# Kernel optimization log

Measured on AMD Instinct MI355X. Metric: run time of the kernel, lower is better.

Reference implementation:

```python
import jax, jax.numpy as jnp
import numpy as np

QMAX = 127.0

def fake_quant(x):
    # per-tensor symmetric int8 fake quantize-dequantize (QAT)
    s = jnp.maximum(jnp.max(jnp.abs(x)) / QMAX, 1e-8)
    q = jnp.clip(jnp.round(x / s), -QMAX, QMAX) * s
    return x + jax.lax.stop_gradient(q - x)  # STE

def qlinear(x, w, b):
    # x already fake-quantized by caller (input_quantizer); weights fake-quantized here
    return jnp.einsum('btc,oc->bto', x, fake_quant(w)) + b

def layer_norm(x, g, b, eps=1e-5):
    m = jnp.mean(x, axis=-1, keepdims=True)
    v = jnp.var(x, axis=-1, keepdims=True)
    return (x - m) * jax.lax.rsqrt(v + eps) * g + b

def setup_inputs() -> dict:
    key = jax.random.key(0)
    ks = jax.random.split(key, 8)
    B, T, C, I = 8, 512, 1024, 4096
    sd = 0.02
    return {
        'hidden_states': jax.random.normal(ks[0], (B, T, C), jnp.float32),
        'attention_mask': jnp.ones((B, T), jnp.float32),
        'ln1_g': jnp.ones((C,), jnp.float32), 'ln1_b': jnp.zeros((C,), jnp.float32),
        'ln2_g': jnp.ones((C,), jnp.float32), 'ln2_b': jnp.zeros((C,), jnp.float32),
        'w_qkv': sd * jax.random.normal(ks[1], (3 * C, C), jnp.float32),
        'b_qkv': jnp.zeros((3 * C,), jnp.float32),
        'w_out': sd * jax.random.normal(ks[2], (C, C), jnp.float32),
        'b_out': jnp.zeros((C,), jnp.float32),
        'w1': sd * jax.random.normal(ks[3], (I, C), jnp.float32),
        'b1': jnp.zeros((I,), jnp.float32),
        'w2': sd * jax.random.normal(ks[4], (C, I), jnp.float32),
        'b2': jnp.zeros((C,), jnp.float32),
    }

def reference(hidden_states, attention_mask, ln1_g, ln1_b, ln2_g, ln2_b,
              w_qkv, b_qkv, w_out, b_out, w1, b1, w2, b2):
    B, T, C = hidden_states.shape
    H = 16
    Dh = C // H
    scale = Dh ** -0.5

    # --- attention branch (pre-norm) ---
    x = layer_norm(hidden_states, ln1_g, ln1_b)
    qkv = qlinear(fake_quant(x), w_qkv, b_qkv)            # [B,T,3C]
    qkv = qkv.reshape(B, T, 3, H, Dh).transpose(2, 0, 3, 1, 4)
    q, k, v = qkv[0], qkv[1], qkv[2]                       # [B,H,T,Dh]
    scores = jnp.einsum('bhqd,bhkd->bhqk', q, k) * scale
    ext = (1.0 - attention_mask)[:, None, None, :] * -10000.0
    scores = scores + ext
    attn = jax.nn.softmax(scores, axis=-1)
    out = jnp.einsum('bhqk,bhkd->bhqd', attn, v)
    out = out.transpose(0, 2, 1, 3).reshape(B, T, C)
    attn_out = qlinear(fake_quant(out), w_out, b_out)
    h = hidden_states + attn_out

    # --- MLP branch (pre-norm) ---
    x = layer_norm(h, ln2_g, ln2_b)
    x = qlinear(fake_quant(x), w1, b1)
    x = jax.nn.gelu(x, approximate=False)
    x = qlinear(fake_quant(x), w2, b2)
    return h + x
```

## Files before the change

### kernel.cpp

```cpp
#include <hip/hip_runtime.h>

typedef __attribute__((ext_vector_type(8))) short bf16x8;
typedef __attribute__((ext_vector_type(4))) float f32x4;
typedef __attribute__((ext_vector_type(4))) int i32x4;
typedef unsigned short u16;
typedef unsigned int u32;

#define B_ 8
#define T_ 512
#define C_ 1024
#define I_ 4096
#define H_ 16
#define Dh_ 64
#define BT (B_*T_)
#define NH (B_*H_)

__device__ __forceinline__ float bf2f(u16 u) {
  return __uint_as_float(((u32)u) << 16);
}
__device__ __forceinline__ u16 f2bf(float f) {
  u32 u = __float_as_uint(f);
  u32 r = u + 0x7FFFu + ((u >> 16) & 1u);
  return (u16)(r >> 16);
}
__device__ __forceinline__ float wredMax(float v) {
#pragma unroll
  for (int o = 32; o; o >>= 1) v = fmaxf(v, __shfl_xor(v, o));
  return v;
}
__device__ __forceinline__ float wredSum(float v) {
#pragma unroll
  for (int o = 32; o; o >>= 1) v += __shfl_xor(v, o);
  return v;
}
__device__ __forceinline__ void slotAtomicMax(u32* arr, int bid, float bm) {
  u32 b = __float_as_uint(bm);
  volatile u32* p = arr + ((bid & 63) << 4);
  if (b > *p) atomicMax((u32*)p, b);
}
__device__ __forceinline__ float slotMax(const u32* __restrict__ arr) {
  float m = 0.f;
#pragma unroll
  for (int i = 0; i < 64; ++i) m = fmaxf(m, __uint_as_float(arr[i << 4]));
  return m;
}
__device__ __forceinline__ void gload16(const void* g, void* l) {
  __builtin_amdgcn_global_load_lds((const __attribute__((address_space(1))) void*)g,
                                   (__attribute__((address_space(3))) void*)l, 16, 0, 0);
}
__device__ __forceinline__ int qi(float v, float inv) {
  return (int)fminf(fmaxf(rintf(v * inv), -127.f), 127.f);
}
__device__ __forceinline__ float gelu1(float v) {
  float x2 = v * v;
  float e = __expf(v * fmaf(-0.0713548755f, x2, -1.5957691216f));
  return v * __builtin_amdgcn_rcpf(1.0f + e);
}

__global__ void k_init(u32* s) {
  int i = blockIdx.x * 256 + threadIdx.x;
  if (i < 8192) s[i] = 0u;
}

__global__ __launch_bounds__(256) void k_pre1(
    const float* __restrict__ p0, int n0,
    const float* __restrict__ p1, int n1,
    const float* __restrict__ p2, int n2,
    const float* __restrict__ p3, int n3,
    u32* __restrict__ scw,
    const float* __restrict__ x, const float* __restrict__ g,
    const float* __restrict__ b, u16* __restrict__ y,
    u32* __restrict__ arr) {
  const int t = threadIdx.x;
  if (blockIdx.x < 512) {
    int stride = 512 * 256;
    int gid = blockIdx.x * 256 + t;
    float m0 = 0.f, m1 = 0.f, m2 = 0.f, m3 = 0.f;
    for (int i = gid; i < n0; i += stride) {
      float4 v = ((const float4*)p0)[i];
      m0 = fmaxf(m0, fmaxf(fmaxf(fabsf(v.x), fabsf(v.y)), fmaxf(fabsf(v.z), fabsf(v.w))));
    }
    for (int i = gid; i < n1; i += stride) {
      float4 v = ((const float4*)p1)[i];
      m1 = fmaxf(m1, fmaxf(fmaxf(fabsf(v.x), fabsf(v.y)), fmaxf(fabsf(v.z), fabsf(v.w))));
    }
    for (int i = gid; i < n2; i += stride) {
      float4 v = ((const float4*)p2)[i];
      m2 = fmaxf(m2, fmaxf(fmaxf(fabsf(v.x), fabsf(v.y)), fmaxf(fabsf(v.z), fabsf(v.w))));
    }
    for (int i = gid; i < n3; i += stride) {
      float4 v = ((const float4*)p3)[i];
      m3 = fmaxf(m3, fmaxf(fmaxf(fabsf(v.x), fabsf(v.y)), fmaxf(fabsf(v.z), fabsf(v.w))));
    }
    m0 = wredMax(m0); m1 = wredMax(m1); m2 = wredMax(m2); m3 = wredMax(m3);
    __shared__ float red4[4][4];
    int wid = t >> 6, lane = t & 63;
    if (lane == 0) { red4[wid][0] = m0; red4[wid][1] = m1; red4[wid][2] = m2; red4[wid][3] = m3; }
    __syncthreads();
    if (t < 4) {
      int j = t;
      float bm = fmaxf(fmaxf(red4[0][j], red4[1][j]), fmaxf(red4[2][j], red4[3][j]));
      slotAtomicMax(scw + j * 1024, blockIdx.x, bm);
    }
  } else {
    int row = blockIdx.x - 512;
    float4 v = ((const float4*)(x + (long)row * C_))[t];
    float s1 = v.x + v.y + v.z + v.w;
    float s2 = v.x * v.x + v.y * v.y + v.z * v.z + v.w * v.w;
    s1 = wredSum(s1);
    s2 = wredSum(s2);
    __shared__ float red[8];
    int wid = t >> 6, lane = t & 63;
    if (lane == 0) { red[wid] = s1; red[4 + wid] = s2; }
    __syncthreads();
    s1 = red[0] + red[1] + red[2] + red[3];
    s2 = red[4] + red[5] + red[6] + red[7];
    float mean = s1 * (1.0f / C_);
    float var = s2 * (1.0f / C_) - mean * mean;
    float inv = rsqrtf(var + 1e-5f);
    float4 gv = ((const float4*)g)[t];
    float4 bv = ((const float4*)b)[t];
    float4 o;
    o.x = (v.x - mean) * inv * gv.x + bv.x;
    o.y = (v.y - mean) * inv * gv.y + bv.y;
    o.z = (v.z - mean) * inv * gv.z + bv.z;
    o.w = (v.w - mean) * inv * gv.w + bv.w;
    ushort4 ob;
    ob.x = f2bf(o.x); ob.y = f2bf(o.y); ob.z = f2bf(o.z); ob.w = f2bf(o.w);
    ((ushort4*)(y + (long)row * C_))[t] = ob;
    float m = fmaxf(fmaxf(fabsf(o.x), fabsf(o.y)), fmaxf(fabsf(o.z), fabsf(o.w)));
    m = wredMax(m);
    __syncthreads();
    if (lane == 0) red[wid] = m;
    __syncthreads();
    if (t == 0) {
      float bm = fmaxf(fmaxf(red[0], red[1]), fmaxf(red[2], red[3]));
      slotAtomicMax(arr, row, bm);
    }
  }
}

__global__ __launch_bounds__(256) void k_pre2(
    const float* __restrict__ p0, signed char* __restrict__ q0, int n0,
    const float* __restrict__ p1, signed char* __restrict__ q1, int n1,
    const float* __restrict__ p2, signed char* __restrict__ q2, int n2,
    const float* __restrict__ p3, signed char* __restrict__ q3, int n3,
    const u32* __restrict__ scw,
    const u16* __restrict__ xb, signed char* __restrict__ xq, int n8,
    const u32* __restrict__ arrX) {
  const int t = threadIdx.x;
  if (blockIdx.x < 512) {
    int stride = 512 * 256;
    int gid = blockIdx.x * 256 + t;
#define QLOOP(p, q, n, slot)                                                        \
    {                                                                               \
      float s = fmaxf(slotMax(scw + slot * 1024) * (1.0f / 127.0f), 1e-8f);         \
      float inv = 1.0f / s;                                                         \
      for (int i = gid; i < n; i += stride) {                                       \
        float4 v = ((const float4*)p)[i];                                           \
        u32 pk = (u32)(qi(v.x, inv) & 255) | ((u32)(qi(v.y, inv) & 255) << 8) |     \
                 ((u32)(qi(v.z, inv) & 255) << 16) | ((u32)(qi(v.w, inv) & 255) << 24); \
        ((u32*)q)[i] = pk;                                                          \
      }                                                                             \
    }
    QLOOP(p0, q0, n0, 0)
    QLOOP(p1, q1, n1, 1)
    QLOOP(p2, q2, n2, 2)
    QLOOP(p3, q3, n3, 3)
#undef QLOOP
  } else {
    float s = fmaxf(slotMax(arrX) * (1.0f / 127.0f), 1e-8f);
    float inv = 1.0f / s;
    int stride = 512 * 256;
    for (int i = (blockIdx.x - 512) * 256 + t; i < n8; i += stride) {
      uint4 d = ((const uint4*)xb)[i];
      u16* e = (u16*)&d;
      uint2 o;
      o.x = (u32)(qi(bf2f(e[0]), inv) & 255) | ((u32)(qi(bf2f(e[1]), inv) & 255) << 8) |
            ((u32)(qi(bf2f(e[2]), inv) & 255) << 16) | ((u32)(qi(bf2f(e[3]), inv) & 255) << 24);
      o.y = (u32)(qi(bf2f(e[4]), inv) & 255) | ((u32)(qi(bf2f(e[5]), inv) & 255) << 8) |
            ((u32)(qi(bf2f(e[6]), inv) & 255) << 16) | ((u32)(qi(bf2f(e[7]), inv) & 255) << 24);
      ((uint2*)xq)[i] = o;
    }
  }
}

__global__ __launch_bounds__(256) void k_quant_b8(const u16* __restrict__ x, signed char* __restrict__ q,
                                                  int n8, const u32* __restrict__ arr) {
  float s = fmaxf(slotMax(arr) * (1.0f / 127.0f), 1e-8f);
  float inv = 1.0f / s;
  int stride = gridDim.x * blockDim.x;
  for (int i = blockIdx.x * blockDim.x + threadIdx.x; i < n8; i += stride) {
    uint4 d = ((const uint4*)x)[i];
    u16* e = (u16*)&d;
    uint2 o;
    o.x = (u32)(qi(bf2f(e[0]), inv) & 255) | ((u32)(qi(bf2f(e[1]), inv) & 255) << 8) |
          ((u32)(qi(bf2f(e[2]), inv) & 255) << 16) | ((u32)(qi(bf2f(e[3]), inv) & 255) << 24);
    o.y = (u32)(qi(bf2f(e[4]), inv) & 255) | ((u32)(qi(bf2f(e[5]), inv) & 255) << 8) |
          ((u32)(qi(bf2f(e[6]), inv) & 255) << 16) | ((u32)(qi(bf2f(e[7]), inv) & 255) << 24);
    ((uint2*)q)[i] = o;
  }
}

__global__ __launch_bounds__(256) void k_lnb(const u16* __restrict__ x, const float* __restrict__ g,
                                             const float* __restrict__ b, u16* __restrict__ y,
                                             u32* __restrict__ arr) {
  int row = blockIdx.x;
  int t = threadIdx.x;
  ushort4 xb = ((const ushort4*)(x + (long)row * C_))[t];
  float4 v;
  v.x = bf2f(xb.x); v.y = bf2f(xb.y); v.z = bf2f(xb.z); v.w = bf2f(xb.w);
  float s1 = v.x + v.y + v.z + v.w;
  float s2 = v.x * v.x + v.y * v.y + v.z * v.z + v.w * v.w;
  s1 = wredSum(s1);
  s2 = wredSum(s2);
  __shared__ float red[8];
  int wid = t >> 6, lane = t & 63;
  if (lane == 0) { red[wid] = s1; red[4 + wid] = s2; }
  __syncthreads();
  s1 = red[0] + red[1] + red[2] + red[3];
  s2 = red[4] + red[5] + red[6] + red[7];
  float mean = s1 * (1.0f / C_);
  float var = s2 * (1.0f / C_) - mean * mean;
  float inv = rsqrtf(var + 1e-5f);
  float4 gv = ((const float4*)g)[t];
  float4 bv = ((const float4*)b)[t];
  float4 o;
  o.x = (v.x - mean) * inv * gv.x + bv.x;
  o.y = (v.y - mean) * inv * gv.y + bv.y;
  o.z = (v.z - mean) * inv * gv.z + bv.z;
  o.w = (v.w - mean) * inv * gv.w + bv.w;
  ushort4 ob;
  ob.x = f2bf(o.x); ob.y = f2bf(o.y); ob.z = f2bf(o.z); ob.w = f2bf(o.w);
  ((ushort4*)(y + (long)row * C_))[t] = ob;
  float m = fmaxf(fmaxf(fabsf(o.x), fabsf(o.y)), fmaxf(fabsf(o.z), fabsf(o.w)));
  m = wredMax(m);
  __syncthreads();
  if (lane == 0) red[wid] = m;
  __syncthreads();
  if (t == 0) {
    float bm = fmaxf(fmaxf(red[0], red[1]), fmaxf(red[2], red[3]));
    slotAtomicMax(arr, row, bm);
  }
}

__global__ __launch_bounds__(256, 1) void k_attn(
    const u16* __restrict__ qkv, const float* __restrict__ mask,
    u16* __restrict__ O, u32* __restrict__ amax) {
  __shared__ u16 Ke[512 * 64];
  __shared__ u16 Vt[64 * 512];
  __shared__ u16 Pl[4 * 64 * 40];
  __shared__ float extl[512];
  __shared__ float redm[4];
  const int tid = threadIdx.x;
  const int w = tid >> 6, l = tid & 63;
  const int head = blockIdx.x;
  const int chunk = blockIdx.y;
  const int b = head >> 4, h = head & 15;
  const long rowbase = (long)(b * 512) * (3 * C_);

  {
    const u16* Kg = qkv + rowbase + C_ + h * 64;
    int lr8 = l >> 3;
    int ls = (l & 7) ^ lr8;
    const long koff = (long)lr8 * (3 * C_) + ls * 8;
#pragma unroll
    for (int i = 0; i < 16; ++i) {
      int r0 = w * 128 + i * 8;
      gload16(Kg + (long)r0 * (3 * C_) + koff, &Ke[r0 * 64]);
    }
  }
  {
    const u16* Vg = qkv + rowbase + 2 * C_ + h * 64;
    int kvl = tid & 31;
    int d0 = (tid >> 5) * 8;
#pragma unroll 4
    for (int i = 0; i < 16; ++i) {
      int kv = i * 32 + kvl;
      uint4 t4 = *(const uint4*)(Vg + (long)kv * (3 * C_) + d0);
      u16* tv = (u16*)&t4;
      int slot = kv >> 3, within = kv & 7;
#pragma unroll
      for (int j = 0; j < 8; ++j) {
        int d = d0 + j;
        Vt[d * 512 + ((slot ^ (d & 7)) << 3) + within] = tv[j];
      }
    }
  }
  {
    const float* mb = mask + b * 512;
    extl[tid] = (1.0f - mb[tid]) * -10000.0f;
    extl[tid + 256] = (1.0f - mb[tid + 256]) * -10000.0f;
  }
  const int qbase = chunk * 256 + w * 64;
  bf16x8 qf[4][2];
  {
    const u16* Qg = qkv + rowbase + h * 64;
#pragma unroll
    for (int qt = 0; qt < 4; ++qt)
#pragma unroll
      for (int dc = 0; dc < 2; ++dc)
        qf[qt][dc] = *(const bf16x8*)(Qg + (long)(qbase + qt * 16 + (l & 15)) * (3 * C_) + dc * 32 + (l >> 4) * 8);
  }
  __syncthreads();

  f32x4 oacc[4][4];
  float mrun[4], lrun[4];
#pragma unroll
  for (int qt = 0; qt < 4; ++qt) { mrun[qt] = -3.0e38f; lrun[qt] = 0.f; }
#pragma unroll
  for (int dt = 0; dt < 4; ++dt)
#pragma unroll
    for (int qt = 0; qt < 4; ++qt) oacc[dt][qt] = (f32x4){0.f, 0.f, 0.f, 0.f};

  u16* Pw = &Pl[w * 64 * 40];

  for (int ks = 0; ks < 16; ++ks) {
    bf16x8 kf[2][2];
#pragma unroll
    for (int kvt = 0; kvt < 2; ++kvt) {
      int kv = ks * 32 + kvt * 16 + (l & 15);
#pragma unroll
      for (int dc = 0; dc < 2; ++dc) {
        int phys = (dc * 4 + (l >> 4)) ^ (kv & 7);
        kf[kvt][dc] = *(const bf16x8*)&Ke[kv * 64 + phys * 8];
      }
    }
    f32x4 sacc[2][4];
#pragma unroll
    for (int kvt = 0; kvt < 2; ++kvt)
#pragma unroll
      for (int qt = 0; qt < 4; ++qt) {
        f32x4 a = (f32x4){0.f, 0.f, 0.f, 0.f};
        a = __builtin_amdgcn_mfma_f32_16x16x32_bf16(kf[kvt][0], qf[qt][0], a, 0, 0, 0);
        a = __builtin_amdgcn_mfma_f32_16x16x32_bf16(kf[kvt][1], qf[qt][1], a, 0, 0, 0);
        sacc[kvt][qt] = a;
      }
#pragma unroll
    for (int kvt = 0; kvt < 2; ++kvt) {
      f32x4 ev = *(const f32x4*)&extl[ks * 32 + kvt * 16 + (l >> 4) * 4];
#pragma unroll
      for (int qt = 0; qt < 4; ++qt)
#pragma unroll
        for (int r = 0; r < 4; ++r)
          sacc[kvt][qt][r] = fmaf(sacc[kvt][qt][r], 0.125f, ev[r]);
    }
#pragma unroll
    for (int qt = 0; qt < 4; ++qt) {
      float pm = sacc[0][qt][0];
#pragma unroll
      for (int r = 1; r < 4; ++r) pm = fmaxf(pm, sacc[0][qt][r]);
#pragma unroll
      for (int r = 0; r < 4; ++r) pm = fmaxf(pm, sacc[1][qt][r]);
      pm = fmaxf(pm, __shfl_xor(pm, 16));
      pm = fmaxf(pm, __shfl_xor(pm, 32));
      float mnew = fmaxf(mrun[qt], pm);
      float f = __expf(mrun[qt] - mnew);
      mrun[qt] = mnew;
      float lsum = 0.f;
#pragma unroll
      for (int kvt = 0; kvt < 2; ++kvt)
#pragma unroll
        for (int r = 0; r < 4; ++r) {
          float p = __expf(sacc[kvt][qt][r] - mnew);
          sacc[kvt][qt][r] = p;
          lsum += p;
        }
      lsum += __shfl_xor(lsum, 16);
      lsum += __shfl_xor(lsum, 32);
      lrun[qt] = lrun[qt] * f + lsum;
#pragma unroll
      for (int dt = 0; dt < 4; ++dt)
#pragma unroll
        for (int r = 0; r < 4; ++r) oacc[dt][qt][r] *= f;
#pragma unroll
      for (int kvt = 0; kvt < 2; ++kvt) {
        u32 p01 = (u32)f2bf(sacc[kvt][qt][0]) | ((u32)f2bf(sacc[kvt][qt][1]) << 16);
        u32 p23 = (u32)f2bf(sacc[kvt][qt][2]) | ((u32)f2bf(sacc[kvt][qt][3]) << 16);
        u16* pr = Pw + (qt * 16 + (l & 15)) * 40 + kvt * 16 + (l >> 4) * 4;
        *(u32*)pr = p01;
        *(u32*)(pr + 2) = p23;
      }
    }
    bf16x8 vf[4], pf[4];
#pragma unroll
    for (int dt = 0; dt < 4; ++dt) {
      int d = dt * 16 + (l & 15);
      int phys = (ks * 4 + (l >> 4)) ^ (d & 7);
      vf[dt] = *(const bf16x8*)&Vt[d * 512 + phys * 8];
    }
#pragma unroll
    for (int qt = 0; qt < 4; ++qt)
      pf[qt] = *(const bf16x8*)(Pw + (qt * 16 + (l & 15)) * 40 + (l >> 4) * 8);
#pragma unroll
    for (int dt = 0; dt < 4; ++dt)
#pragma unroll
      for (int qt = 0; qt < 4; ++qt)
        oacc[dt][qt] = __builtin_amdgcn_mfma_f32_16x16x32_bf16(vf[dt], pf[qt], oacc[dt][qt], 0, 0, 0);
  }

  float lmax = 0.f;
  u16* Ob = O + (long)(b * 512 + qbase) * C_ + h * 64;
#pragma unroll
  for (int qt = 0; qt < 4; ++qt) {
    float inv = 1.0f / lrun[qt];
    long qoff = (long)(qt * 16 + (l & 15)) * C_;
#pragma unroll
    for (int dt = 0; dt < 4; ++dt) {
      int d = dt * 16 + (l >> 4) * 4;
      float v0 = oacc[dt][qt][0] * inv;
      float v1 = oacc[dt][qt][1] * inv;
      float v2 = oacc[dt][qt][2] * inv;
      float v3 = oacc[dt][qt][3] * inv;
      lmax = fmaxf(fmaxf(lmax, fmaxf(fabsf(v0), fabsf(v1))), fmaxf(fabsf(v2), fabsf(v3)));
      u32 a01 = (u32)f2bf(v0) | ((u32)f2bf(v1) << 16);
      u32 a23 = (u32)f2bf(v2) | ((u32)f2bf(v3) << 16);
      *(u32*)(Ob + qoff + d) = a01;
      *(u32*)(Ob + qoff + d + 2) = a23;
    }
  }
  lmax = wredMax(lmax);
  if (l == 0) redm[w] = lmax;
  __syncthreads();
  if (tid == 0)
    slotAtomicMax(amax, blockIdx.x * 2 + blockIdx.y,
                  fmaxf(fmaxf(redm[0], redm[1]), fmaxf(redm[2], redm[3])));
}

template <int BM, int BN, int EPI, bool SWZ>
__global__ __launch_bounds__(256) void k_gemmq(
    const signed char* __restrict__ A, int lda,
    const signed char* __restrict__ Bm, int ldb,
    const float* __restrict__ bias,
    void* __restrict__ Cp, int ldc,
    int M, int N, int K,
    const void* __restrict__ resid,
    u32* __restrict__ amaxOut,
    const u32* __restrict__ amaxA, const u32* __restrict__ amaxB) {
  constexpr int BK = 128;
  constexpr int MF = (BM / 2) / 16;
  constexpr int NF = (BN / 2) / 16;
  constexpr int NLD = BM / 32 + BN / 32;
  __shared__ __align__(16) signed char As[2][BM * BK];
  __shared__ __align__(16) signed char Bs[2][BN * BK];
  const int tid = threadIdx.x;
  const int wid = tid >> 6, lane = tid & 63;
  const int wr = wid >> 1, wc = wid & 1;

  float sa = fmaxf(slotMax(amaxA) * (1.0f / 127.0f), 1e-8f);
  float sb = fmaxf(slotMax(amaxB) * (1.0f / 127.0f), 1e-8f);
  const float sAB = sa * sb;

  int bx = blockIdx.x, by = blockIdx.y;
  if (SWZ) {
    int gx = gridDim.x;
    int nwg = gx * gridDim.y;
    int bid = by * gx + bx;
    int cpx = nwg >> 3;
    int swz = (bid & 7) * cpx + (bid >> 3);
    bx = swz % gx;
    by = swz / gx;
  }

  const signed char* Ab = A + (long)by * BM * lda;
  const signed char* Bb = Bm + (long)bx * BN * ldb;

  i32x4 acc[MF][NF];
#pragma unroll
  for (int m = 0; m < MF; m++)
#pragma unroll
    for (int n = 0; n < NF; n++) acc[m][n] = (i32x4){0, 0, 0, 0};

  const int lr = lane & 15;
  const int l8 = lane >> 3;
  const int s8 = (lane & 7) ^ l8;
  const long aoff = (long)l8 * lda + s8 * 16;
  const long boff = (long)l8 * ldb + s8 * 16;

  auto stageAB = [&](int buf, int k0) {
#pragma unroll
    for (int i = 0; i < BM / 32; ++i) {
      int R0 = wid * (BM / 4) + i * 8;
      gload16(Ab + (long)R0 * lda + k0 + aoff, &As[buf][R0 * BK]);
    }
#pragma unroll
    for (int i = 0; i < BN / 32; ++i) {
      int R0 = wid * (BN / 4) + i * 8;
      gload16(Bb + (long)R0 * ldb + k0 + boff, &Bs[buf][R0 * BK]);
    }
  };

  auto waitCounted = [&]() {
    if constexpr (NLD == 8) {
      asm volatile("s_waitcnt vmcnt(8)" ::: "memory");
    } else if constexpr (NLD == 6) {
      asm volatile("s_waitcnt vmcnt(6)" ::: "memory");
    } else {
      asm volatile("s_waitcnt vmcnt(4)" ::: "memory");
    }
  };

  auto computeK = [&](int buf) {
#pragma unroll
    for (int kk = 0; kk < 2; ++kk) {
      const int sl = (kk << 2) + (lane >> 4);
      const int sf = (sl ^ (lr & 7)) << 4;
      i32x4 af[MF], bfr[NF];
#pragma unroll
      for (int m = 0; m < MF; m++)
        af[m] = *(const i32x4*)&As[buf][(wr * (BM / 2) + m * 16 + lr) * BK + sf];
#pragma unroll
      for (int n = 0; n < NF; n++)
        bfr[n] = *(const i32x4*)&Bs[buf][(wc * (BN / 2) + n * 16 + lr) * BK + sf];
      __builtin_amdgcn_s_setprio(1);
#pragma unroll
      for (int m = 0; m < MF; m++)
#pragma unroll
        for (int n = 0; n < NF; n++)
          acc[m][n] = __builtin_amdgcn_mfma_i32_16x16x64_i8(af[m], bfr[n], acc[m][n], 0, 0, 0);
      __builtin_amdgcn_s_setprio(0);
    }
  };

  const int nt = K / BK;
  stageAB(0, 0);
  int cur = 0;
  for (int t = 0; t < nt; ++t) {
    if (t + 1 < nt) {
      stageAB(cur ^ 1, (t + 1) * BK);
      waitCounted();
    } else {
      asm volatile("s_waitcnt vmcnt(0)" ::: "memory");
    }
    __builtin_amdgcn_s_barrier();
    computeK(cur);
    if (t + 1 < nt)
      __builtin_amdgcn_s_barrier();
    cur ^= 1;
  }

  const int rowBase = by * BM + wr * (BM / 2);
  const int colBase = bx * BN + wc * (BN / 2);
  float lmax = 0.f;
#pragma unroll
  for (int m = 0; m < MF; m++) {
    int row0 = rowBase + m * 16 + (lane >> 4) * 4;
#pragma unroll
    for (int n = 0; n < NF; n++) {
      int col = colBase + n * 16 + lr;
      float bs = bias[col];
#pragma unroll
      for (int j = 0; j < 4; j++) {
        int row = row0 + j;
        long idx = (long)row * ldc + col;
        float v = (float)acc[m][n][j] * sAB;
        if (EPI == 0) {
          ((u16*)Cp)[idx] = f2bf(v + bs);
        } else if (EPI == 1) {
          ((u16*)Cp)[idx] = f2bf(v + bs + ((const float*)resid)[idx]);
        } else if (EPI == 2) {
          v = gelu1(v + bs);
          lmax = fmaxf(fmaxf(lmax, v), 0.0f - v);
          ((u16*)Cp)[idx] = f2bf(v);
        } else if (EPI == 3) {
          ((float*)Cp)[idx] = v + bs + bf2f(((const u16*)resid)[idx]);
        }
      }
    }
  }
  if (EPI == 2) {
    __shared__ float redm[4];
    float wm = wredMax(lmax);
    if (lane == 0) redm[wid] = wm;
    __syncthreads();
    if (tid == 0) {
      float bm = fmaxf(fmaxf(redm[0], redm[1]), fmaxf(redm[2], redm[3]));
      slotAtomicMax(amaxOut, blockIdx.y * gridDim.x + blockIdx.x, bm);
    }
  }
}

__global__ __launch_bounds__(512, 1) void k_gemmq8(
    const signed char* __restrict__ A, int lda,
    const signed char* __restrict__ Bm, int ldb,
    const float* __restrict__ bias,
    u16* __restrict__ Cp, int ldc,
    int K,
    u32* __restrict__ amaxOut,
    const u32* __restrict__ amaxA, const u32* __restrict__ amaxB) {
  __shared__ __align__(16) signed char As[2][256 * 128];
  __shared__ __align__(16) signed char Bs[2][256 * 128];
  const int tid = threadIdx.x;
  const int wid = tid >> 6, lane = tid & 63;
  const int wr = wid >> 2, wc = wid & 3;
  const int lr = lane & 15;

  float sa = fmaxf(slotMax(amaxA) * (1.0f / 127.0f), 1e-8f);
  float sb = fmaxf(slotMax(amaxB) * (1.0f / 127.0f), 1e-8f);
  const float sAB = sa * sb;

  int bx = blockIdx.x, by = blockIdx.y;
  {
    int bid = by * 16 + bx;
    int swz = (bid & 7) * 32 + (bid >> 3);
    bx = swz & 15;
    by = swz >> 4;
  }
  const signed char* Ab = A + (long)by * 256 * lda;
  const signed char* Bb = Bm + (long)bx * 256 * ldb;

  i32x4 acc[8][4];
#pragma unroll
  for (int m = 0; m < 8; m++)
#pragma unroll
    for (int n = 0; n < 4; n++) acc[m][n] = (i32x4){0, 0, 0, 0};

  const int l8 = lane >> 3;
  const int s8 = (lane & 7) ^ l8;
  const long aoff = (long)l8 * lda + s8 * 16;
  const long boff = (long)l8 * ldb + s8 * 16;

  auto stageHalf = [&](int buf, int kt, int h) {
    int k0 = kt * 128;
    if (h < 2) {
      int R0 = h * 128 + wid * 16;
      gload16(Ab + (long)R0 * lda + k0 + aoff, &As[buf][R0 * 128]);
      gload16(Ab + (long)(R0 + 8) * lda + k0 + aoff, &As[buf][(R0 + 8) * 128]);
    } else {
      int R0 = (h - 2) * 128 + wid * 16;
      gload16(Bb + (long)R0 * ldb + k0 + boff, &Bs[buf][R0 * 128]);
      gload16(Bb + (long)(R0 + 8) * ldb + k0 + boff, &Bs[buf][(R0 + 8) * 128]);
    }
  };

  const int nt = K / 128;
#define PHASE(BUF, MH, KS, STAGESTMT)                                              \
  {                                                                                \
    const int slotl = (KS) * 4 + (lane >> 4);                                      \
    i32x4 af[4], bfr[4];                                                           \
    _Pragma("unroll") for (int i = 0; i < 4; ++i) {                                \
      int row = wr * 128 + ((MH) * 4 + i) * 16 + lr;                               \
      af[i] = *(const i32x4*)&As[BUF][row * 128 + ((slotl ^ (row & 7)) << 4)];     \
    }                                                                              \
    _Pragma("unroll") for (int n = 0; n < 4; ++n) {                                \
      int row = wc * 64 + n * 16 + lr;                                             \
      bfr[n] = *(const i32x4*)&Bs[BUF][row * 128 + ((slotl ^ (row & 7)) << 4)];    \
    }                                                                              \
    STAGESTMT;                                                                     \
    __builtin_amdgcn_s_barrier();                                                  \
    __builtin_amdgcn_s_setprio(1);                                                 \
    _Pragma("unroll") for (int i = 0; i < 4; ++i)                                  \
      _Pragma("unroll") for (int n = 0; n < 4; ++n)                                \
        acc[(MH) * 4 + i][n] =                                                     \
            __builtin_amdgcn_mfma_i32_16x16x64_i8(af[i], bfr[n], acc[(MH) * 4 + i][n], 0, 0, 0); \
    __builtin_amdgcn_s_setprio(0);                                                 \
    __builtin_amdgcn_s_barrier();                                                  \
  }

  stageHalf(0, 0, 0);
  stageHalf(0, 0, 2);
  stageHalf(0, 0, 3);
  stageHalf(0, 0, 1);

  int cur = 0;
  for (int t = 0; t < nt; ++t) {
    const bool stg = (t + 1 < nt);
    const int nb = cur ^ 1;
    const int tn = t + 1;
    asm volatile("s_waitcnt vmcnt(2)" ::: "memory");
    __builtin_amdgcn_s_barrier();
    PHASE(cur, 0, 0, { if (stg) stageHalf(nb, tn, 0); })
    PHASE(cur, 0, 1, { if (stg) stageHalf(nb, tn, 2); })
    if (stg) {
      asm volatile("s_waitcnt vmcnt(4)" ::: "memory");
    } else {
      asm volatile("s_waitcnt vmcnt(0)" ::: "memory");
    }
    __builtin_amdgcn_s_barrier();
    PHASE(cur, 1, 0, { if (stg) stageHalf(nb, tn, 3); })
    PHASE(cur, 1, 1, { if (stg) stageHalf(nb, tn, 1); })
    cur = nb;
  }
#undef PHASE

  const int rowBase = by * 256 + wr * 128;
  const int colBase = bx * 256 + wc * 64;
  float lmax = 0.f;
#pragma unroll
  for (int m = 0; m < 8; m++) {
    int row0 = rowBase + m * 16 + (lane >> 4) * 4;
#pragma unroll
    for (int n = 0; n < 4; n++) {
      int col = colBase + n * 16 + lr;
      float bs = bias[col];
#pragma unroll
      for (int j = 0; j < 4; j++) {
        long idx = (long)(row0 + j) * ldc + col;
        float v = gelu1((float)acc[m][n][j] * sAB + bs);
        lmax = fmaxf(fmaxf(lmax, v), 0.0f - v);
        Cp[idx] = f2bf(v);
      }
    }
  }
  {
    __shared__ float redm[8];
    float wm = wredMax(lmax);
    if (lane == 0) redm[wid] = wm;
    __syncthreads();
    if (tid == 0) {
      float bm = redm[0];
#pragma unroll
      for (int i = 1; i < 8; ++i) bm = fmaxf(bm, redm[i]);
      slotAtomicMax(amaxOut, blockIdx.y * gridDim.x + blockIdx.x, bm);
    }
  }
}

extern "C" void kernel_launch(void* const* d_in, const int* in_sizes, int n_in,
                              void* d_out, int out_size, void* d_ws, size_t ws_size,
                              hipStream_t stream) {
  const float* hidden = (const float*)d_in[0];
  const float* mask = (const float*)d_in[1];
  const float* ln1g = (const float*)d_in[2];
  const float* ln1b = (const float*)d_in[3];
  const float* ln2g = (const float*)d_in[4];
  const float* ln2b = (const float*)d_in[5];
  const float* w_qkv = (const float*)d_in[6];
  const float* b_qkv = (const float*)d_in[7];
  const float* w_out = (const float*)d_in[8];
  const float* b_out = (const float*)d_in[9];
  const float* w1 = (const float*)d_in[10];
  const float* b1 = (const float*)d_in[11];
  const float* w2 = (const float*)d_in[12];
  const float* b2 = (const float*)d_in[13];

  char* ws = (char*)d_ws;
  u32* sc = (u32*)ws;
  const long MB = 1024 * 1024;
  signed char* wq_qkv = (signed char*)(ws + 1 * MB);
  signed char* wq_out = (signed char*)(ws + 4 * MB);
  signed char* wq_w1  = (signed char*)(ws + 6 * MB);
  signed char* wq_w2  = (signed char*)(ws + 10 * MB);
  signed char* xq     = (signed char*)(ws + 14 * MB);
  u16* x1             = (u16*)(ws + 18 * MB);
  signed char* Oq     = (signed char*)(ws + 26 * MB);
  u16* O              = (u16*)(ws + 30 * MB);
  u16* qkv            = (u16*)(ws + 38 * MB);
  u16* hbuf           = (u16*)(ws + 62 * MB);
  u16* y1             = (u16*)(ws + 78 * MB);
  signed char* y1q    = (signed char*)(ws + 110 * MB);

  k_init<<<32, 256, 0, stream>>>(sc);

  k_pre1<<<512 + BT, 256, 0, stream>>>(
      w_qkv, 3 * C_ * C_ / 4, w_out, C_ * C_ / 4, w1, I_ * C_ / 4, w2, C_ * I_ / 4, sc,
      hidden, ln1g, ln1b, x1, sc + 4 * 1024);

  k_pre2<<<1024, 256, 0, stream>>>(
      w_qkv, wq_qkv, 3 * C_ * C_ / 4, w_out, wq_out, C_ * C_ / 4,
      w1, wq_w1, I_ * C_ / 4, w2, wq_w2, C_ * I_ / 4, sc,
      x1, xq, BT * C_ / 8, sc + 4 * 1024);

  k_gemmq<128, 128, 0, true><<<dim3(24, 32), 256, 0, stream>>>(
      xq, C_, wq_qkv, C_, b_qkv, qkv, 3 * C_,
      BT, 3 * C_, C_, nullptr, nullptr, sc + 4 * 1024, sc + 0 * 1024);

  k_attn<<<dim3(NH, 2), 256, 0, stream>>>(qkv, mask, O, sc + 5 * 1024);
  k_quant_b8<<<512, 256, 0, stream>>>(O, Oq, BT * C_ / 8, sc + 5 * 1024);

  k_gemmq<64, 64, 1, true><<<dim3(16, 64), 256, 0, stream>>>(
      Oq, C_, wq_out, C_, b_out, hbuf, C_,
      BT, C_, C_, hidden, nullptr, sc + 5 * 1024, sc + 1 * 1024);

  k_lnb<<<BT, 256, 0, stream>>>(hbuf, ln2g, ln2b, x1, sc + 6 * 1024);
  k_quant_b8<<<512, 256, 0, stream>>>(x1, xq, BT * C_ / 8, sc + 6 * 1024);

  k_gemmq8<<<dim3(16, 16), 512, 0, stream>>>(
      xq, C_, wq_w1, C_, b1, y1, I_, C_,
      sc + 7 * 1024, sc + 6 * 1024, sc + 2 * 1024);
  k_quant_b8<<<512, 256, 0, stream>>>(y1, y1q, BT * I_ / 8, sc + 7 * 1024);

  k_gemmq<64, 64, 3, true><<<dim3(16, 64), 256, 0, stream>>>(
      y1q, I_, wq_w2, I_, b2, d_out, C_,
      BT, C_, I_, hbuf, nullptr, sc + 7 * 1024, sc + 3 * 1024);
}
```

Before: 238.7 us.

## Fuse int8 quantization into attention and FC1 kernels via grid barrier

Adds an in-kernel grid-wide barrier (atomic counter spin-wait) to the attention and FC1 GEMM kernels. After every block has published its abs-max, each block reads the global max and quantizes its own output tile to int8, so the separate k_quant_b8 launches for O and y1 go away. This saves two kernel launches and lets the quantize pass re-read data the same block just wrote, which is likely still in cache. It depends on all 256 blocks being resident at once, otherwise the barrier deadlocks, and it also removes the unused EPI==2 path from the generic GEMM.

```diff
diff --git a/kernel.cpp b/kernel.cpp
--- a/kernel.cpp
+++ b/kernel.cpp
@@ -44,6 +44,23 @@
   for (int i = 0; i < 64; ++i) m = fmaxf(m, __uint_as_float(arr[i << 4]));
   return m;
 }
+__device__ __forceinline__ float slotMaxAcq(const u32* __restrict__ arr) {
+  float m = 0.f;
+#pragma unroll
+  for (int i = 0; i < 64; ++i) {
+    u32 v = __hip_atomic_load(arr + (i << 4), __ATOMIC_RELAXED, __HIP_MEMORY_SCOPE_AGENT);
+    m = fmaxf(m, __uint_as_float(v));
+  }
+  return m;
+}
+__device__ __forceinline__ void gridBarrier(u32* ctr, u32 n) {
+  __hip_atomic_fetch_add(ctr, 1u, __ATOMIC_ACQ_REL, __HIP_MEMORY_SCOPE_AGENT);
+  u32 v;
+  do {
+    v = __hip_atomic_load(ctr, __ATOMIC_ACQUIRE, __HIP_MEMORY_SCOPE_AGENT);
+    if (v < n) __builtin_amdgcn_s_sleep(8);
+  } while (v < n);
+}
 __device__ __forceinline__ void gload16(const void* g, void* l) {
   __builtin_amdgcn_global_load_lds((const __attribute__((address_space(1))) void*)g,
                                    (__attribute__((address_space(3))) void*)l, 16, 0, 0);
@@ -59,7 +76,7 @@
 
 __global__ void k_init(u32* s) {
   int i = blockIdx.x * 256 + threadIdx.x;
-  if (i < 8192) s[i] = 0u;
+  if (i < 8704) s[i] = 0u;
 }
 
 __global__ __launch_bounds__(256) void k_pre1(
@@ -246,7 +263,8 @@
 
 __global__ __launch_bounds__(256, 1) void k_attn(
     const u16* __restrict__ qkv, const float* __restrict__ mask,
-    u16* __restrict__ O, u32* __restrict__ amax) {
+    u16* __restrict__ O, u32* __restrict__ amax,
+    signed char* __restrict__ Oq, u32* __restrict__ ctr) {
   __shared__ u16 Ke[512 * 64];
   __shared__ u16 Vt[64 * 512];
   __shared__ u16 Pl[4 * 64 * 40];
@@ -421,10 +439,32 @@
   }
   lmax = wredMax(lmax);
   if (l == 0) redm[w] = lmax;
+  __threadfence();
   __syncthreads();
-  if (tid == 0)
+  if (tid == 0) {
     slotAtomicMax(amax, blockIdx.x * 2 + blockIdx.y,
                   fmaxf(fmaxf(redm[0], redm[1]), fmaxf(redm[2], redm[3])));
+    gridBarrier(ctr, 256u);
+  }
+  __syncthreads();
+  {
+    float s = fmaxf(slotMaxAcq(amax) * (1.0f / 127.0f), 1e-8f);
+    float invq = 1.0f / s;
+    const long base = (long)(b * 512 + chunk * 256) * C_ + h * 64;
+#pragma unroll
+    for (int i = 0; i < 8; ++i) {
+      int e = (tid + i * 256) * 8;
+      int r = e >> 6, c = e & 63;
+      uint4 d = *(const uint4*)(O + base + (long)r * C_ + c);
+      u16* el = (u16*)&d;
+      uint2 o;
+      o.x = (u32)(qi(bf2f(el[0]), invq) & 255) | ((u32)(qi(bf2f(el[1]), invq) & 255) << 8) |
+            ((u32)(qi(bf2f(el[2]), invq) & 255) << 16) | ((u32)(qi(bf2f(el[3]), invq) & 255) << 24);
+      o.y = (u32)(qi(bf2f(el[4]), invq) & 255) | ((u32)(qi(bf2f(el[5]), invq) & 255) << 8) |
+            ((u32)(qi(bf2f(el[6]), invq) & 255) << 16) | ((u32)(qi(bf2f(el[7]), invq) & 255) << 24);
+      *(uint2*)(Oq + base + (long)r * C_ + c) = o;
+    }
+  }
 }
 
 template <int BM, int BN, int EPI, bool SWZ>
@@ -541,7 +581,6 @@
 
   const int rowBase = by * BM + wr * (BM / 2);
   const int colBase = bx * BN + wc * (BN / 2);
-  float lmax = 0.f;
 #pragma unroll
   for (int m = 0; m < MF; m++) {
     int row0 = rowBase + m * 16 + (lane >> 4) * 4;
@@ -558,24 +597,10 @@
           ((u16*)Cp)[idx] = f2bf(v + bs);
         } else if (EPI == 1) {
           ((u16*)Cp)[idx] = f2bf(v + bs + ((const float*)resid)[idx]);
-        } else if (EPI == 2) {
-          v = gelu1(v + bs);
-          lmax = fmaxf(fmaxf(lmax, v), 0.0f - v);
-          ((u16*)Cp)[idx] = f2bf(v);
         } else if (EPI == 3) {
           ((float*)Cp)[idx] = v + bs + bf2f(((const u16*)resid)[idx]);
         }
       }
-    }
-  }
-  if (EPI == 2) {
-    __shared__ float redm[4];
-    float wm = wredMax(lmax);
-    if (lane == 0) redm[wid] = wm;
-    __syncthreads();
-    if (tid == 0) {
-      float bm = fmaxf(fmaxf(redm[0], redm[1]), fmaxf(redm[2], redm[3]));
-      slotAtomicMax(amaxOut, blockIdx.y * gridDim.x + blockIdx.x, bm);
     }
   }
 }
@@ -587,7 +612,8 @@
     u16* __restrict__ Cp, int ldc,
     int K,
     u32* __restrict__ amaxOut,
-    const u32* __restrict__ amaxA, const u32* __restrict__ amaxB) {
+    const u32* __restrict__ amaxA, const u32* __restrict__ amaxB,
+    signed char* __restrict__ Cq, u32* __restrict__ ctr) {
   __shared__ __align__(16) signed char As[2][256 * 128];
   __shared__ __align__(16) signed char Bs[2][256 * 128];
   const int tid = threadIdx.x;
@@ -706,12 +732,33 @@
     __shared__ float redm[8];
     float wm = wredMax(lmax);
     if (lane == 0) redm[wid] = wm;
+    __threadfence();
     __syncthreads();
     if (tid == 0) {
       float bm = redm[0];
 #pragma unroll
       for (int i = 1; i < 8; ++i) bm = fmaxf(bm, redm[i]);
       slotAtomicMax(amaxOut, blockIdx.y * gridDim.x + blockIdx.x, bm);
+      gridBarrier(ctr, 256u);
+    }
+    __syncthreads();
+  }
+  {
+    float s = fmaxf(slotMaxAcq(amaxOut) * (1.0f / 127.0f), 1e-8f);
+    float invq = 1.0f / s;
+    const long base = (long)(by * 256) * ldc + bx * 256;
+#pragma unroll
+    for (int i = 0; i < 16; ++i) {
+      int e = (tid + i * 512) * 8;
+      int r = e >> 8, c = e & 255;
+      uint4 d = *(const uint4*)(Cp + base + (long)r * ldc + c);
+      u16* el = (u16*)&d;
+      uint2 o;
+      o.x = (u32)(qi(bf2f(el[0]), invq) & 255) | ((u32)(qi(bf2f(el[1]), invq) & 255) << 8) |
+            ((u32)(qi(bf2f(el[2]), invq) & 255) << 16) | ((u32)(qi(bf2f(el[3]), invq) & 255) << 24);
+      o.y = (u32)(qi(bf2f(el[4]), invq) & 255) | ((u32)(qi(bf2f(el[5]), invq) & 255) << 8) |
+            ((u32)(qi(bf2f(el[6]), invq) & 255) << 16) | ((u32)(qi(bf2f(el[7]), invq) & 255) << 24);
+      *(uint2*)(Cq + base + (long)r * ldc + c) = o;
     }
   }
 }
@@ -736,6 +783,8 @@
 
   char* ws = (char*)d_ws;
   u32* sc = (u32*)ws;
+  u32* ctrA = sc + 8192;
+  u32* ctrW = sc + 8208;
   const long MB = 1024 * 1024;
   signed char* wq_qkv = (signed char*)(ws + 1 * MB);
   signed char* wq_out = (signed char*)(ws + 4 * MB);
@@ -750,7 +799,7 @@
   u16* y1             = (u16*)(ws + 78 * MB);
   signed char* y1q    = (signed char*)(ws + 110 * MB);
 
-  k_init<<<32, 256, 0, stream>>>(sc);
+  k_init<<<34, 256, 0, stream>>>(sc);
 
   k_pre1<<<512 + BT, 256, 0, stream>>>(
       w_qkv, 3 * C_ * C_ / 4, w_out, C_ * C_ / 4, w1, I_ * C_ / 4, w2, C_ * I_ / 4, sc,
@@ -765,8 +814,7 @@
       xq, C_, wq_qkv, C_, b_qkv, qkv, 3 * C_,
       BT, 3 * C_, C_, nullptr, nullptr, sc + 4 * 1024, sc + 0 * 1024);
 
-  k_attn<<<dim3(NH, 2), 256, 0, stream>>>(qkv, mask, O, sc + 5 * 1024);
-  k_quant_b8<<<512, 256, 0, stream>>>(O, Oq, BT * C_ / 8, sc + 5 * 1024);
+  k_attn<<<dim3(NH, 2), 256, 0, stream>>>(qkv, mask, O, sc + 5 * 1024, Oq, ctrA);
 
   k_gemmq<64, 64, 1, true><<<dim3(16, 64), 256, 0, stream>>>(
       Oq, C_, wq_out, C_, b_out, hbuf, C_,
@@ -777,8 +825,7 @@
 
   k_gemmq8<<<dim3(16, 16), 512, 0, stream>>>(
       xq, C_, wq_w1, C_, b1, y1, I_, C_,
-      sc + 7 * 1024, sc + 6 * 1024, sc + 2 * 1024);
-  k_quant_b8<<<512, 256, 0, stream>>>(y1, y1q, BT * I_ / 8, sc + 7 * 1024);
+      sc + 7 * 1024, sc + 6 * 1024, sc + 2 * 1024, y1q, ctrW);
 
   k_gemmq<64, 64, 3, true><<<dim3(16, 64), 256, 0, stream>>>(
       y1q, I_, wq_w2, I_, b2, d_out, C_,
```

New measurement: 359.4 us. 50.5% more time.
